# Kernel optimization log

Hardware: AMD Instinct MI355X
Metric: run time of the kernel (lower is better)

Reference implementation:

```python
import jax, jax.numpy as jnp
import numpy as np

B, T, D = 4, 2048, 1024

def setup_inputs() -> dict:
    key = jax.random.key(0)
    kx, kq, kk, kv = jax.random.split(key, 4)
    lim = 1.0 / np.sqrt(D)
    x = jax.random.normal(kx, (B, T, D), dtype=jnp.float32)
    # nn.Linear weights (stored as [out,in]); applied as x @ W.T
    W_q = jax.random.uniform(kq, (D, D), jnp.float32, -lim, lim)
    W_k = jax.random.uniform(kk, (D, D), jnp.float32, -lim, lim)
    W_v = jax.random.uniform(kv, (D, D), jnp.float32, -lim, lim)
    return {"x": x, "W_q": W_q, "W_k": W_k, "W_v": W_v}

def reference(x, W_q, W_k, W_v):
    d = x.shape[-1]
    Q = jnp.einsum('btd,ed->bte', x, W_q)
    K = jnp.einsum('btd,ed->bte', x, W_k)
    V = jnp.einsum('btd,ed->bte', x, W_v)
    att = jnp.einsum('bqd,bkd->bqk', Q, K) / jnp.sqrt(jnp.asarray(d, x.dtype))
    weights = jax.nn.softmax(att, axis=-1)  # NOTE: original applies no causal mask
    return jnp.einsum('bqk,bkd->bqd', weights, V)
```

## Files before the change

### kernel.cpp

```cpp
#include <hip/hip_runtime.h>
#include <hip/hip_bf16.h>
#include <math.h>
#include <type_traits>


typedef short shortx8 __attribute__((ext_vector_type(8)));
typedef short shortx4 __attribute__((ext_vector_type(4)));
typedef float floatx16 __attribute__((ext_vector_type(16)));
typedef __attribute__((address_space(3))) void lds_void_t;
typedef __attribute__((address_space(1))) const void gmem_void_t;

#define GLD16(gp, lp) \
    __builtin_amdgcn_global_load_lds((gmem_void_t*)(gp), (lds_void_t*)(lp), 16, 0, 0)

#define MODE_PROJ 0
#define MODE_EXP  1
#define MODE_DIV  2

template <int MODE>
__global__ __launch_bounds__(256) void mfma_gemm_abt(
    const __hip_bfloat16* __restrict__ A, const __hip_bfloat16* __restrict__ B,
    void* __restrict__ Cv, float* __restrict__ rowsum,
    __hip_bfloat16* __restrict__ Vt,
    int M, int N, int K, long sA, long sB, long sC, float alpha)
{
    __shared__ __hip_bfloat16 As[128 * 32];
    __shared__ __hip_bfloat16 Bs[128 * 32];

    using CT = std::conditional_t<MODE == MODE_DIV, float, __hip_bfloat16>;

    const int z = blockIdx.z;
    A += (long)z * sA;
    B += (long)z * sB;
    CT* C = (CT*)Cv + (long)z * sC;

    const int t     = threadIdx.x;
    const int wave  = t >> 6;
    const int lane  = t & 63;
    const int m0    = blockIdx.x * 128;
    const int n0    = blockIdx.y * 128;
    const int wm    = (wave >> 1) * 64;
    const int wn    = (wave & 1) * 64;
    const int lrow  = lane & 31;
    const int lhalf = lane >> 5;

    const int srow = t >> 2;
    const int scol = (t & 3) * 8;

    floatx16 acc[2][2] = {};

    for (int k0 = 0; k0 < K; k0 += 32) {
        GLD16(A + (long)(m0 + srow) * K + k0 + scol,      As + wave * 512);
        GLD16(A + (long)(m0 + 64 + srow) * K + k0 + scol, As + 2048 + wave * 512);
        GLD16(B + (long)(n0 + srow) * K + k0 + scol,      Bs + wave * 512);
        GLD16(B + (long)(n0 + 64 + srow) * K + k0 + scol, Bs + 2048 + wave * 512);
        __syncthreads();

        #pragma unroll
        for (int h = 0; h < 2; ++h) {
            shortx8 af[2], bf[2];
            #pragma unroll
            for (int i = 0; i < 2; ++i)
                af[i] = *(const shortx8*)(As + (wm + 32 * i + lrow) * 32 + h * 16 + lhalf * 8);
            #pragma unroll
            for (int j = 0; j < 2; ++j)
                bf[j] = *(const shortx8*)(Bs + (wn + 32 * j + lrow) * 32 + h * 16 + lhalf * 8);
            #pragma unroll
            for (int i = 0; i < 2; ++i)
                #pragma unroll
                for (int j = 0; j < 2; ++j)
                    acc[i][j] = __builtin_amdgcn_mfma_f32_32x32x16_bf16(
                        af[i], bf[j], acc[i][j], 0, 0, 0);
        }
        __syncthreads();
    }

    if constexpr (MODE == MODE_PROJ) {
        if (z == 2) {
            const int bz   = m0 >> 11;
            const long bo  = (long)bz * N * 2048;
            #pragma unroll
            for (int i = 0; i < 2; ++i)
                #pragma unroll
                for (int j = 0; j < 2; ++j)
                    #pragma unroll
                    for (int g = 0; g < 4; ++g) {
                        const int trow = (m0 + wm + 32 * i + g * 8 + 4 * lhalf) & 2047;
                        const long col = n0 + wn + 32 * j + lrow;
                        shortx4 pk;
                        #pragma unroll
                        for (int r = 0; r < 4; ++r) {
                            __hip_bfloat16 hb = __float2bfloat16(acc[i][j][4 * g + r]);
                            pk[r] = *(short*)&hb;
                        }
                        *(shortx4*)(Vt + bo + col * 2048 + trow) = pk;
                    }
        } else {
            #pragma unroll
            for (int i = 0; i < 2; ++i)
                #pragma unroll
                for (int j = 0; j < 2; ++j)
                    #pragma unroll
                    for (int g = 0; g < 4; ++g)
                        #pragma unroll
                        for (int r = 0; r < 4; ++r) {
                            const long row = m0 + wm + 32 * i + g * 8 + 4 * lhalf + r;
                            const long col = n0 + wn + 32 * j + lrow;
                            C[row * N + col] = __float2bfloat16(acc[i][j][4 * g + r]);
                        }
        }
    } else if constexpr (MODE == MODE_EXP) {
        #pragma unroll
        for (int i = 0; i < 2; ++i) {
            float rs[16];
            #pragma unroll
            for (int reg = 0; reg < 16; ++reg) rs[reg] = 0.0f;
            #pragma unroll
            for (int j = 0; j < 2; ++j)
                #pragma unroll
                for (int g = 0; g < 4; ++g)
                    #pragma unroll
                    for (int r = 0; r < 4; ++r) {
                        const long row = m0 + wm + 32 * i + g * 8 + 4 * lhalf + r;
                        const long col = n0 + wn + 32 * j + lrow;
                        const float e = __expf(acc[i][j][4 * g + r] * alpha);
                        rs[4 * g + r] += e;
                        C[row * N + col] = __float2bfloat16(e);
                    }
            #pragma unroll
            for (int reg = 0; reg < 16; ++reg) {
                float v = rs[reg];
                v += __shfl_xor(v, 1);
                v += __shfl_xor(v, 2);
                v += __shfl_xor(v, 4);
                v += __shfl_xor(v, 8);
                v += __shfl_xor(v, 16);
                if (lrow == 0) {
                    const long row = m0 + wm + 32 * i + (reg >> 2) * 8 + 4 * lhalf + (reg & 3);
                    atomicAdd(&rowsum[(long)z * M + row], v);
                }
            }
        }
    } else {
        #pragma unroll
        for (int i = 0; i < 2; ++i) {
            float inv[16];
            #pragma unroll
            for (int g = 0; g < 4; ++g)
                #pragma unroll
                for (int r = 0; r < 4; ++r) {
                    const long row = m0 + wm + 32 * i + g * 8 + 4 * lhalf + r;
                    inv[4 * g + r] = 1.0f / rowsum[(long)z * M + row];
                }
            #pragma unroll
            for (int j = 0; j < 2; ++j)
                #pragma unroll
                for (int g = 0; g < 4; ++g)
                    #pragma unroll
                    for (int r = 0; r < 4; ++r) {
                        const long row = m0 + wm + 32 * i + g * 8 + 4 * lhalf + r;
                        const long col = n0 + wn + 32 * j + lrow;
                        C[row * N + col] = acc[i][j][4 * g + r] * inv[4 * g + r];
                    }
        }
    }
}

__global__ __launch_bounds__(256) void cast_f32_bf16(
    const float* __restrict__ in, __hip_bfloat16* __restrict__ out, int n4)
{
    const int i = blockIdx.x * 256 + threadIdx.x;
    if (i < n4) {
        const float4 f = ((const float4*)in)[i];
        out[i * 4 + 0] = __float2bfloat16(f.x);
        out[i * 4 + 1] = __float2bfloat16(f.y);
        out[i * 4 + 2] = __float2bfloat16(f.z);
        out[i * 4 + 3] = __float2bfloat16(f.w);
    }
}

__global__ __launch_bounds__(256) void cast_w3_f32_bf16(
    const float* __restrict__ W0, const float* __restrict__ W1,
    const float* __restrict__ W2, __hip_bfloat16* __restrict__ out, int n4)
{
    const int y = blockIdx.y;
    const float* src = (y == 0) ? W0 : (y == 1) ? W1 : W2;
    __hip_bfloat16* dst = out + (long)y * n4 * 4;
    const int i = blockIdx.x * 256 + threadIdx.x;
    if (i < n4) {
        const float4 f = ((const float4*)src)[i];
        dst[i * 4 + 0] = __float2bfloat16(f.x);
        dst[i * 4 + 1] = __float2bfloat16(f.y);
        dst[i * 4 + 2] = __float2bfloat16(f.z);
        dst[i * 4 + 3] = __float2bfloat16(f.w);
    }
}

extern "C" void kernel_launch(void* const* d_in, const int* in_sizes, int n_in,
                              void* d_out, int out_size, void* d_ws, size_t ws_size,
                              hipStream_t stream)
{
    constexpr int  Bb = 4, T = 2048, D = 1024;
    constexpr int  M  = Bb * T;
    constexpr long TD = (long)T * D;
    constexpr long TT = (long)T * T;
    constexpr long MD = (long)M * D;

    const float* x  = (const float*)d_in[0];
    const float* Wq = (const float*)d_in[1];
    const float* Wk = (const float*)d_in[2];
    const float* Wv = (const float*)d_in[3];
    float* out = (float*)d_out;

    __hip_bfloat16* Q  = (__hip_bfloat16*)d_ws;
    __hip_bfloat16* Kb = Q + MD;
    __hip_bfloat16* Vt = Kb + MD;
    __hip_bfloat16* P  = Vt + MD;
    __hip_bfloat16* xb = P + (long)Bb * TT;
    __hip_bfloat16* Wb = xb + MD;
    float*     rowsum  = (float*)(Wb + 3L * D * D);

    dim3 blk(256);

    (void)hipMemsetAsync(rowsum, 0, (size_t)Bb * T * sizeof(float), stream);

    cast_f32_bf16<<<dim3(MD / 4 / 256), blk, 0, stream>>>(x, xb, MD / 4);
    cast_w3_f32_bf16<<<dim3((D * D) / 4 / 256, 3), blk, 0, stream>>>(
        Wq, Wk, Wv, Wb, D * D / 4);

    mfma_gemm_abt<MODE_PROJ><<<dim3(M / 128, D / 128, 3), blk, 0, stream>>>(
        xb, Wb, Q, nullptr, Vt, M, D, D, 0, (long)D * D, MD, 1.0f);

    mfma_gemm_abt<MODE_EXP><<<dim3(T / 128, T / 128, Bb), blk, 0, stream>>>(
        Q, Kb, P, rowsum, nullptr, T, T, D, TD, TD, TT, 0.03125f);

    mfma_gemm_abt<MODE_DIV><<<dim3(T / 128, D / 128, Bb), blk, 0, stream>>>(
        P, Vt, out, rowsum, nullptr, T, D, T, TT, TD, TD, 1.0f);

    (void)in_sizes; (void)n_in; (void)out_size; (void)ws_size;
}
```

Before: 295.2 us.

## Swizzle LDS tile layout and fuse cast/memset prep into one kernel

Applies an XOR swizzle to the 16-byte chunk column used when staging A/B tiles into LDS via global_load_lds, and the matching swizzle on the MFMA fragment reads, to reduce LDS bank conflicts in all three GEMMs. It also merges the x cast, the three weight casts and the rowsum memset into a single prep kernel to cut launch overhead. The swizzle must match exactly between writers and readers, or the GEMM inputs will be scrambled.

After: 278.8 us. 1.06x faster.

```diff
diff --git a/kernel.cpp b/kernel.cpp
--- a/kernel.cpp
+++ b/kernel.cpp
@@ -45,7 +45,10 @@
     const int lhalf = lane >> 5;
 
     const int srow = t >> 2;
-    const int scol = (t & 3) * 8;
+    const int fs   = ((t >> 2) & 3) ^ ((t >> 4) & 1);
+    const int scol = (((t & 3) ^ fs)) * 8;
+
+    const int fr = (lrow & 3) ^ ((lrow >> 2) & 1);
 
     floatx16 acc[2][2] = {};
 
@@ -58,13 +61,14 @@
 
         #pragma unroll
         for (int h = 0; h < 2; ++h) {
+            const int koff = (((2 * h + lhalf) ^ fr)) * 8;
             shortx8 af[2], bf[2];
             #pragma unroll
             for (int i = 0; i < 2; ++i)
-                af[i] = *(const shortx8*)(As + (wm + 32 * i + lrow) * 32 + h * 16 + lhalf * 8);
+                af[i] = *(const shortx8*)(As + (wm + 32 * i + lrow) * 32 + koff);
             #pragma unroll
             for (int j = 0; j < 2; ++j)
-                bf[j] = *(const shortx8*)(Bs + (wn + 32 * j + lrow) * 32 + h * 16 + lhalf * 8);
+                bf[j] = *(const shortx8*)(Bs + (wn + 32 * j + lrow) * 32 + koff);
             #pragma unroll
             for (int i = 0; i < 2; ++i)
                 #pragma unroll
@@ -166,34 +170,35 @@
     }
 }
 
-__global__ __launch_bounds__(256) void cast_f32_bf16(
-    const float* __restrict__ in, __hip_bfloat16* __restrict__ out, int n4)
+__global__ __launch_bounds__(256) void prep(
+    const float* __restrict__ x,
+    const float* __restrict__ W0, const float* __restrict__ W1,
+    const float* __restrict__ W2,
+    __hip_bfloat16* __restrict__ xb, __hip_bfloat16* __restrict__ Wb,
+    float* __restrict__ rowsum, int n4x, int n4w)
 {
-    const int i = blockIdx.x * 256 + threadIdx.x;
-    if (i < n4) {
-        const float4 f = ((const float4*)in)[i];
-        out[i * 4 + 0] = __float2bfloat16(f.x);
-        out[i * 4 + 1] = __float2bfloat16(f.y);
-        out[i * 4 + 2] = __float2bfloat16(f.z);
-        out[i * 4 + 3] = __float2bfloat16(f.w);
-    }
-}
-
-__global__ __launch_bounds__(256) void cast_w3_f32_bf16(
-    const float* __restrict__ W0, const float* __restrict__ W1,
-    const float* __restrict__ W2, __hip_bfloat16* __restrict__ out, int n4)
-{
-    const int y = blockIdx.y;
-    const float* src = (y == 0) ? W0 : (y == 1) ? W1 : W2;
-    __hip_bfloat16* dst = out + (long)y * n4 * 4;
-    const int i = blockIdx.x * 256 + threadIdx.x;
-    if (i < n4) {
-        const float4 f = ((const float4*)src)[i];
-        dst[i * 4 + 0] = __float2bfloat16(f.x);
-        dst[i * 4 + 1] = __float2bfloat16(f.y);
-        dst[i * 4 + 2] = __float2bfloat16(f.z);
-        dst[i * 4 + 3] = __float2bfloat16(f.w);
-    }
+    const long i = (long)blockIdx.x * 256 + threadIdx.x;
+    if (i < 2048) {
+        float4 zz; zz.x = zz.y = zz.z = zz.w = 0.0f;
+        ((float4*)rowsum)[i] = zz;
+    }
+    const float* src;
+    __hip_bfloat16* dst;
+    long j;
+    if (i < n4x) {
+        src = x; dst = xb; j = i;
+    } else {
+        const long k = i - n4x;
+        const int w  = (int)(k >> 18);
+        j = k & (n4w - 1);
+        src = (w == 0) ? W0 : (w == 1) ? W1 : W2;
+        dst = Wb + (long)w * n4w * 4;
+    }
+    const float4 f = ((const float4*)src)[j];
+    dst[j * 4 + 0] = __float2bfloat16(f.x);
+    dst[j * 4 + 1] = __float2bfloat16(f.y);
+    dst[j * 4 + 2] = __float2bfloat16(f.z);
+    dst[j * 4 + 3] = __float2bfloat16(f.w);
 }
 
 extern "C" void kernel_launch(void* const* d_in, const int* in_sizes, int n_in,
@@ -222,11 +227,10 @@
 
     dim3 blk(256);
 
-    (void)hipMemsetAsync(rowsum, 0, (size_t)Bb * T * sizeof(float), stream);
-
-    cast_f32_bf16<<<dim3(MD / 4 / 256), blk, 0, stream>>>(x, xb, MD / 4);
-    cast_w3_f32_bf16<<<dim3((D * D) / 4 / 256, 3), blk, 0, stream>>>(
-        Wq, Wk, Wv, Wb, D * D / 4);
+    constexpr int n4x = (int)(MD / 4);
+    constexpr int n4w = D * D / 4;
+    prep<<<dim3((n4x + 3 * n4w) / 256), blk, 0, stream>>>(
+        x, Wq, Wk, Wv, xb, Wb, rowsum, n4x, n4w);
 
     mfma_gemm_abt<MODE_PROJ><<<dim3(M / 128, D / 128, 3), blk, 0, stream>>>(
         xb, Wb, Q, nullptr, Vt, M, D, D, 0, (long)D * D, MD, 1.0f);
```
